# Kernel tuning notes

Measured on AMD Instinct MI355X. Metric: run time of the kernel, lower is better.

## Reference

```python
import jax, jax.numpy as jnp
import numpy as np
from math import sqrt

B, S, D, H = 4, 2048, 1024, 16
DH = D // H          # 64
DF = 4 * D           # 4096
EPS = 1e-5
NEG = -1e9


def layer_norm(x, w, b):
    mu = jnp.mean(x, axis=-1, keepdims=True)
    var = jnp.mean((x - mu) ** 2, axis=-1, keepdims=True)
    return (x - mu) * jax.lax.rsqrt(var + EPS) * w + b


def setup_inputs() -> dict:
    key = jax.random.key(0)
    ks = jax.random.split(key, 16)
    s = 0.02
    return {
        "state": jax.random.normal(ks[0], (B, S, D), jnp.float32),
        "mask": jax.random.randint(ks[1], (B, S), 0, 2, jnp.int32),
        "ln1_w": jnp.ones((D,), jnp.float32),
        "ln1_b": jnp.zeros((D,), jnp.float32),
        "Wq": jax.random.normal(ks[2], (H, D, DH), jnp.float32) * s,
        "bq": jnp.zeros((H, DH), jnp.float32),
        "Wk": jax.random.normal(ks[3], (H, D, DH), jnp.float32) * s,
        "bk": jnp.zeros((H, DH), jnp.float32),
        "Wv": jax.random.normal(ks[4], (H, D, DH), jnp.float32) * s,
        "bv": jnp.zeros((H, DH), jnp.float32),
        "Wo": jax.random.normal(ks[5], (D, D), jnp.float32) * s,
        "bo": jnp.zeros((D,), jnp.float32),
        "ln2_w": jnp.ones((D,), jnp.float32),
        "ln2_b": jnp.zeros((D,), jnp.float32),
        "W1": jax.random.normal(ks[6], (D, DF), jnp.float32) * s,
        "b1": jnp.zeros((DF,), jnp.float32),
        "W2": jax.random.normal(ks[7], (DF, D), jnp.float32) * s,
        "b2": jnp.zeros((D,), jnp.float32),
    }


def reference(state, mask, ln1_w, ln1_b, Wq, bq, Wk, bk, Wv, bv, Wo, bo,
              ln2_w, ln2_b, W1, b1, W2, b2):
    # pre-norm attention block
    hidden = layer_norm(state, ln1_w, ln1_b)               # [B,S,D]
    q = jnp.einsum("bsd,hde->bhse", hidden, Wq) + bq[None, :, None, :]
    k = jnp.einsum("bsd,hde->bhse", hidden, Wk) + bk[None, :, None, :]
    v = jnp.einsum("bsd,hde->bhse", hidden, Wv) + bv[None, :, None, :]
    scores = jnp.einsum("bhse,bhte->bhst", q, k) / sqrt(DH)  # [B,H,S,S]
    scores = jnp.where(mask[:, None, None, :] == 0, NEG, scores)
    weights = jax.nn.softmax(scores, axis=-1)
    attended = jnp.einsum("bhst,bhte->bhse", weights, v)    # [B,H,S,DH]
    # concat heads in head order (matches torch cat over per-head outputs)
    attended = attended.transpose(0, 2, 1, 3).reshape(B, S, D)
    attn_out = attended @ Wo + bo
    output = state + attn_out
    # pre-norm FFN block (dropout=0 -> identity)
    hidden = layer_norm(output, ln2_w, ln2_b)
    ff = jax.nn.gelu(hidden @ W1 + b1, approximate=False) @ W2 + b2
    return output + ff
```

## Files before the change

### kernel.cpp

```cpp
#include <hip/hip_runtime.h>
#include <math.h>

#define B_  4
#define S_  2048
#define D_  1024
#define H_  16
#define DH_ 64
#define DF_ 4096
#define M_  8192

typedef __attribute__((ext_vector_type(8))) short bf8_t;
typedef __attribute__((ext_vector_type(4))) short bf4_t;
typedef __attribute__((ext_vector_type(4))) float f4_t;

__device__ __forceinline__ unsigned short f2bf(float x) {
  union { float f; unsigned u; } v; v.f = x;
  unsigned r = v.u + 0x7fffu + ((v.u >> 16) & 1u);
  return (unsigned short)(r >> 16);
}

#if defined(__has_builtin)
#if __has_builtin(__builtin_amdgcn_cvt_pk_bf16_f32)
#define HAVE_PKCVT 1
#endif
#if __has_builtin(__builtin_amdgcn_mfma_f32_16x16x16bf16_1k)
#define HAVE_MFMA16 1
#endif
#if __has_builtin(__builtin_amdgcn_global_load_lds)
#define HAVE_ASYNC 1
#endif
#endif

__device__ __forceinline__ unsigned pk_bf16(float lo, float hi) {
#ifdef HAVE_PKCVT
  auto r = __builtin_amdgcn_cvt_pk_bf16_f32(lo, hi);
  unsigned u; __builtin_memcpy(&u, &r, 4); return u;
#else
  return (unsigned)f2bf(lo) | ((unsigned)f2bf(hi) << 16);
#endif
}

__device__ __forceinline__ bf4_t upk(unsigned u0, unsigned u1) {
  union { unsigned u[2]; bf4_t v; } c; c.u[0] = u0; c.u[1] = u1; return c.v;
}

__device__ __forceinline__ f4_t mfma32(bf8_t a, bf8_t b, f4_t c) {
  return __builtin_amdgcn_mfma_f32_16x16x32_bf16(a, b, c, 0, 0, 0);
}

__device__ __forceinline__ f4_t mfma16(bf4_t a, bf4_t b, f4_t c) {
#ifdef HAVE_MFMA16
  return __builtin_amdgcn_mfma_f32_16x16x16bf16_1k(a, b, c, 0, 0, 0);
#else
  bf8_t a8 = {a[0], a[1], a[2], a[3], 0, 0, 0, 0};
  bf8_t b8 = {b[0], b[1], b[2], b[3], 0, 0, 0, 0};
  return __builtin_amdgcn_mfma_f32_16x16x32_bf16(a8, b8, c, 0, 0, 0);
#endif
}

__device__ __forceinline__ void async16(const void* g, void* l) {
#ifdef HAVE_ASYNC
  __builtin_amdgcn_global_load_lds((__attribute__((address_space(1))) void*)(g),
                                   (__attribute__((address_space(3))) void*)(l), 16, 0, 0);
#else
  *(uint4*)l = *(const uint4*)g;
#endif
}

__device__ __forceinline__ int sw(int row) { return (row ^ (row >> 3)) & 7; }


__global__ __launch_bounds__(256) void wtrans_kernel(const float* __restrict__ in,
                                                     unsigned short* __restrict__ out,
                                                     int K, int N) {
  const int k0 = blockIdx.x * 32, n0 = blockIdx.y * 32;
  __shared__ float t[32][33];
  const int tid = threadIdx.x;
#pragma unroll
  for (int i = 0; i < 4; i++) {
    int idx = i * 256 + tid; int r = idx >> 5, c = idx & 31;
    t[r][c] = in[(size_t)(k0 + r) * N + n0 + c];
  }
  __syncthreads();
#pragma unroll
  for (int i = 0; i < 4; i++) {
    int idx = i * 256 + tid; int r = idx >> 5, c = idx & 31;
    out[(size_t)(n0 + r) * K + k0 + c] = f2bf(t[c][r]);
  }
}

__global__ __launch_bounds__(256) void qkvpack_kernel(const float* __restrict__ Wq,
                                                      const float* __restrict__ Wk,
                                                      const float* __restrict__ Wv,
                                                      unsigned short* __restrict__ WqkvT) {
  const int z = blockIdx.z;
  const int sel = z >> 4, h = z & 15;
  const float* in = (sel == 0 ? Wq : sel == 1 ? Wk : Wv) + (size_t)h * D_ * DH_;
  const int k0 = blockIdx.x * 32, n0 = blockIdx.y * 32;
  __shared__ float t[32][33];
  const int tid = threadIdx.x;
#pragma unroll
  for (int i = 0; i < 4; i++) {
    int idx = i * 256 + tid; int r = idx >> 5, c = idx & 31;
    t[r][c] = in[(size_t)(k0 + r) * DH_ + n0 + c];
  }
  __syncthreads();
#pragma unroll
  for (int i = 0; i < 4; i++) {
    int idx = i * 256 + tid; int r = idx >> 5, c = idx & 31;
    int n = sel * 1024 + h * 64 + n0 + r;
    WqkvT[(size_t)n * D_ + k0 + c] = f2bf(t[c][r]);
  }
}

__global__ void biaspack_kernel(const float* __restrict__ bq, const float* __restrict__ bk,
                                const float* __restrict__ bv, float* __restrict__ bqkv) {
  int i = blockIdx.x * 256 + threadIdx.x;
  if (i < 3072) {
    int sel = i >> 10, j = i & 1023;
    const float* src = sel == 0 ? bq : sel == 1 ? bk : bv;
    bqkv[i] = src[j];
  }
}


__global__ __launch_bounds__(256) void ln_kernel(const float* __restrict__ x,
                                                 const float* __restrict__ w,
                                                 const float* __restrict__ bb,
                                                 unsigned short* __restrict__ out) {
  const int row = blockIdx.x;
  const float* xr = x + (size_t)row * D_;
  const int tid = threadIdx.x;
  float v[4]; float s = 0.f;
#pragma unroll
  for (int i = 0; i < 4; i++) { v[i] = xr[tid + i * 256]; s += v[i]; }
  __shared__ float red[8];
#pragma unroll
  for (int o = 32; o; o >>= 1) s += __shfl_xor(s, o, 64);
  const int wv = tid >> 6, ln = tid & 63;
  if (!ln) red[wv] = s;
  __syncthreads();
  float mean = (red[0] + red[1] + red[2] + red[3]) * (1.f / 1024.f);
  float s2 = 0.f;
#pragma unroll
  for (int i = 0; i < 4; i++) { float d = v[i] - mean; s2 += d * d; }
#pragma unroll
  for (int o = 32; o; o >>= 1) s2 += __shfl_xor(s2, o, 64);
  if (!ln) red[4 + wv] = s2;
  __syncthreads();
  float var = (red[4] + red[5] + red[6] + red[7]) * (1.f / 1024.f);
  float rstd = rsqrtf(var + 1e-5f);
#pragma unroll
  for (int i = 0; i < 4; i++) {
    int c = tid + i * 256;
    out[(size_t)row * D_ + c] = f2bf((v[i] - mean) * rstd * w[c] + bb[c]);
  }
}

template <int EPI>
__global__ __launch_bounds__(256) void gemm_bt(const unsigned short* __restrict__ A,
                                               const unsigned short* __restrict__ Bt,
                                               const float* __restrict__ bias,
                                               const float* __restrict__ resid,
                                               unsigned short* __restrict__ outb,
                                               float* __restrict__ outf,
                                               int Ndim, int Kdim) {
  __shared__ __align__(16) unsigned short Asmem[4096];
  __shared__ __align__(16) unsigned short Bsmem[4096];
  const int tid = threadIdx.x;
  const int wave = tid >> 6, lane = tid & 63;
  const int quad = lane >> 4, l16 = lane & 15;
  const int wm = wave >> 1, wn = wave & 1;
  const int m0 = blockIdx.y * 128, n0 = blockIdx.x * 128;

  const f4_t fzero = {0.f, 0.f, 0.f, 0.f};
  f4_t acc[4][4];
#pragma unroll
  for (int i = 0; i < 4; i++)
#pragma unroll
    for (int j = 0; j < 4; j++) acc[i][j] = fzero;

  const int rowA = tid >> 2;
  const int kp = (tid & 3) * 8;

  for (int k0 = 0; k0 < Kdim; k0 += 32) {
    __syncthreads();
#pragma unroll
    for (int r = 0; r < 2; r++) {
      const int row = r * 64 + rowA;
      const int e = row * 32 + kp;
      async16(A  + (size_t)(m0 + row) * Kdim + k0 + kp, &Asmem[e]);
      async16(Bt + (size_t)(n0 + row) * Kdim + k0 + kp, &Bsmem[e]);
    }
    __syncthreads();

    bf8_t a[4], b[4];
#pragma unroll
    for (int i = 0; i < 4; i++) {
      a[i] = *(const bf8_t*)&Asmem[(wm * 64 + i * 16 + l16) * 32 + quad * 8];
      b[i] = *(const bf8_t*)&Bsmem[(wn * 64 + i * 16 + l16) * 32 + quad * 8];
    }
#pragma unroll
    for (int i = 0; i < 4; i++)
#pragma unroll
      for (int j = 0; j < 4; j++)
        acc[i][j] = mfma32(a[i], b[j], acc[i][j]);
  }

#pragma unroll
  for (int i = 0; i < 4; i++) {
#pragma unroll
    for (int j = 0; j < 4; j++) {
#pragma unroll
      for (int r = 0; r < 4; r++) {
        const int m = m0 + wm * 64 + i * 16 + quad * 4 + r;
        const int n = n0 + wn * 64 + j * 16 + l16;
        float v = acc[i][j][r] + bias[n];
        if constexpr (EPI == 2) v = 0.5f * v * (1.f + erff(v * 0.70710678118654752f));
        if constexpr (EPI == 1) {
          v += resid[(size_t)m * Ndim + n];
          outf[(size_t)m * Ndim + n] = v;
        } else {
          outb[(size_t)m * Ndim + n] = f2bf(v);
        }
      }
    }
  }
}


__global__ __launch_bounds__(256) void vtrans_kernel(const unsigned short* __restrict__ qkv,
                                                     unsigned short* __restrict__ vT) {
  const int bh = blockIdx.y, b = bh >> 4, h = bh & 15;
  const int t0 = blockIdx.x * 64;
  __shared__ unsigned short tile[64][65];
  const int tid = threadIdx.x;
#pragma unroll
  for (int i = 0; i < 16; i++) {
    int idx = i * 256 + tid;
    int t = idx >> 6, e = idx & 63;
    tile[e][t] = qkv[(size_t)(b * S_ + t0 + t) * 3072 + 2048 + h * 64 + e];
  }
  __syncthreads();
#pragma unroll
  for (int i = 0; i < 16; i++) {
    int idx = i * 256 + tid;
    int e = idx >> 6, t = idx & 63;
    vT[(size_t)(bh * 64 + e) * S_ + t0 + t] = tile[e][t];
  }
}


__global__ __launch_bounds__(256) void attn_kernel(const unsigned short* __restrict__ qkv,
                                                   const unsigned short* __restrict__ vT,
                                                   const int* __restrict__ maskp,
                                                   unsigned short* __restrict__ attended) {
  const int bh = blockIdx.y, b = bh >> 4, h = bh & 15;
  const int q0 = blockIdx.x * 128;
  const int tid = threadIdx.x, wv = tid >> 6, lane = tid & 63;
  const int quad = lane >> 4, l16 = lane & 15;
  __shared__ __align__(16) unsigned short smem[16640];
  __shared__ float biasl[64];
  unsigned short* Qs = smem;
  unsigned short* Ks = smem + 8192;
  unsigned short* Vs = smem + 12288;

#pragma unroll
  for (int r = 0; r < 4; r++) {
    int ci = r * 256 + tid;
    int row = ci >> 3, lc = (ci & 7) ^ sw(row);
    async16(qkv + (size_t)(b * S_ + q0 + row) * 3072 + h * 64 + lc * 8, &Qs[ci * 8]);
  }
  __syncthreads();
  bf8_t aq[2][2];
#pragma unroll
  for (int sb = 0; sb < 2; sb++) {
    int srow = wv * 32 + sb * 16 + l16;
    int sq = sw(srow);
    aq[sb][0] = *(const bf8_t*)&Qs[srow * 64 + (quad ^ sq) * 8];
    aq[sb][1] = *(const bf8_t*)&Qs[srow * 64 + ((quad + 4) ^ sq) * 8];
  }

  const f4_t fzero = {0.f, 0.f, 0.f, 0.f};
  f4_t o[2][4];
#pragma unroll
  for (int sb = 0; sb < 2; sb++)
#pragma unroll
    for (int ee = 0; ee < 4; ee++) o[sb][ee] = fzero;
  float lsum[2] = {0.f, 0.f};

  for (int t0 = 0; t0 < S_; t0 += 64) {
    __syncthreads();
#pragma unroll
    for (int r = 0; r < 2; r++) {
      int ci = r * 256 + tid;
      int row = ci >> 3, lc = (ci & 7) ^ sw(row);
      async16(qkv + (size_t)(b * S_ + t0 + row) * 3072 + 1024 + h * 64 + lc * 8, &Ks[ci * 8]);
      async16(vT + (size_t)(bh * 64 + row) * S_ + t0 + lc * 8, &Vs[ci * 8]);
    }
    if (tid < 64) biasl[tid] = maskp[b * S_ + t0 + tid] ? 0.f : -8e9f;
    __syncthreads();

    f4_t sf[2][4];
#pragma unroll
    for (int jj = 0; jj < 4; jj++) {
      f4_t bi = *(const f4_t*)&biasl[jj * 16 + quad * 4];
      sf[0][jj] = bi;
      sf[1][jj] = bi;
    }
#pragma unroll
    for (int jj = 0; jj < 4; jj++) {
      int krow = jj * 16 + l16, sk = sw(krow);
      bf8_t kf0 = *(const bf8_t*)&Ks[krow * 64 + (quad ^ sk) * 8];
      bf8_t kf1 = *(const bf8_t*)&Ks[krow * 64 + ((quad + 4) ^ sk) * 8];
      sf[0][jj] = mfma32(kf0, aq[0][0], sf[0][jj]);
      sf[0][jj] = mfma32(kf1, aq[0][1], sf[0][jj]);
      sf[1][jj] = mfma32(kf0, aq[1][0], sf[1][jj]);
      sf[1][jj] = mfma32(kf1, aq[1][1], sf[1][jj]);
    }

    unsigned pk[2][4][2];
#pragma unroll
    for (int sb = 0; sb < 2; sb++)
#pragma unroll
      for (int jj = 0; jj < 4; jj++) {
        float p0 = __expf(sf[sb][jj][0] * 0.125f);
        float p1 = __expf(sf[sb][jj][1] * 0.125f);
        float p2 = __expf(sf[sb][jj][2] * 0.125f);
        float p3 = __expf(sf[sb][jj][3] * 0.125f);
        lsum[sb] += (p0 + p1) + (p2 + p3);
        pk[sb][jj][0] = pk_bf16(p0, p1);
        pk[sb][jj][1] = pk_bf16(p2, p3);
      }

#pragma unroll
    for (int ee = 0; ee < 4; ee++) {
      int vrow = ee * 16 + l16, sv = sw(vrow);
#pragma unroll
      for (int jj = 0; jj < 4; jj++) {
        int lc2 = 2 * jj + (quad >> 1);
        bf4_t vf = *(const bf4_t*)&Vs[vrow * 64 + (lc2 ^ sv) * 8 + (quad & 1) * 4];
        o[0][ee] = mfma16(vf, upk(pk[0][jj][0], pk[0][jj][1]), o[0][ee]);
        o[1][ee] = mfma16(vf, upk(pk[1][jj][0], pk[1][jj][1]), o[1][ee]);
      }
    }
  }

#pragma unroll
  for (int sb = 0; sb < 2; sb++) {
    float l = lsum[sb];
    l += __shfl_xor(l, 16, 64);
    l += __shfl_xor(l, 32, 64);
    lsum[sb] = 1.f / l;
  }

  __syncthreads();
  unsigned short* Os = smem;
#pragma unroll
  for (int sb = 0; sb < 2; sb++) {
    int srow = wv * 32 + sb * 16 + l16;
#pragma unroll
    for (int ee = 0; ee < 4; ee++) {
      unsigned w0 = pk_bf16(o[sb][ee][0] * lsum[sb], o[sb][ee][1] * lsum[sb]);
      unsigned w1 = pk_bf16(o[sb][ee][2] * lsum[sb], o[sb][ee][3] * lsum[sb]);
      uint2 wq; wq.x = w0; wq.y = w1;
      *(uint2*)&Os[srow * 72 + ee * 16 + quad * 4] = wq;
    }
  }
  __syncthreads();
#pragma unroll
  for (int it = 0; it < 4; it++) {
    int row = it * 32 + (tid >> 3), e0 = (tid & 7) * 8;
    bf8_t v = *(const bf8_t*)&Os[row * 72 + e0];
    *(bf8_t*)&attended[(size_t)(b * S_ + q0 + row) * D_ + h * 64 + e0] = v;
  }
}


extern "C" void kernel_launch(void* const* d_in, const int* in_sizes, int n_in,
                              void* d_out, int out_size, void* d_ws, size_t ws_size,
                              hipStream_t stream) {
  const float* state = (const float*)d_in[0];
  const int*   maskp = (const int*)d_in[1];
  const float* ln1w  = (const float*)d_in[2];
  const float* ln1b  = (const float*)d_in[3];
  const float* Wq    = (const float*)d_in[4];
  const float* bq    = (const float*)d_in[5];
  const float* Wk    = (const float*)d_in[6];
  const float* bk    = (const float*)d_in[7];
  const float* Wv    = (const float*)d_in[8];
  const float* bv    = (const float*)d_in[9];
  const float* Wo    = (const float*)d_in[10];
  const float* bo    = (const float*)d_in[11];
  const float* ln2w  = (const float*)d_in[12];
  const float* ln2b  = (const float*)d_in[13];
  const float* W1    = (const float*)d_in[14];
  const float* b1    = (const float*)d_in[15];
  const float* W2    = (const float*)d_in[16];
  const float* b2    = (const float*)d_in[17];

  char* w = (char*)d_ws;
  unsigned short* hidden = (unsigned short*)w; w += (size_t)M_ * D_ * 2;
  unsigned short* qkv    = (unsigned short*)w; w += (size_t)M_ * 3072 * 2;
  unsigned short* vT     = (unsigned short*)w; w += (size_t)M_ * D_ * 2;
  float*          outp   = (float*)w;          w += (size_t)M_ * D_ * 4;
  unsigned short* WqkvT  = (unsigned short*)w; w += (size_t)3072 * D_ * 2;
  unsigned short* WoT    = (unsigned short*)w; w += (size_t)D_ * D_ * 2;
  unsigned short* W1T    = (unsigned short*)w; w += (size_t)DF_ * D_ * 2;
  unsigned short* W2T    = (unsigned short*)w; w += (size_t)D_ * DF_ * 2;
  float*          bqkv   = (float*)w;          w += 3072 * 4;
  unsigned short* ff1    = qkv;

  qkvpack_kernel<<<dim3(32, 2, 48), 256, 0, stream>>>(Wq, Wk, Wv, WqkvT);
  wtrans_kernel<<<dim3(32, 32), 256, 0, stream>>>(Wo, WoT, D_, D_);
  wtrans_kernel<<<dim3(32, 128), 256, 0, stream>>>(W1, W1T, D_, DF_);
  wtrans_kernel<<<dim3(128, 32), 256, 0, stream>>>(W2, W2T, DF_, D_);
  biaspack_kernel<<<12, 256, 0, stream>>>(bq, bk, bv, bqkv);

  ln_kernel<<<M_, 256, 0, stream>>>(state, ln1w, ln1b, hidden);
  gemm_bt<0><<<dim3(3072 / 128, M_ / 128), 256, 0, stream>>>(hidden, WqkvT, bqkv, nullptr,
                                                             qkv, nullptr, 3072, D_);
  vtrans_kernel<<<dim3(S_ / 64, B_ * H_), 256, 0, stream>>>(qkv, vT);
  attn_kernel<<<dim3(S_ / 128, B_ * H_), 256, 0, stream>>>(qkv, vT, maskp, hidden);
  gemm_bt<1><<<dim3(D_ / 128, M_ / 128), 256, 0, stream>>>(hidden, WoT, bo, state,
                                                           nullptr, outp, D_, D_);
  ln_kernel<<<M_, 256, 0, stream>>>(outp, ln2w, ln2b, hidden);
  gemm_bt<2><<<dim3(DF_ / 128, M_ / 128), 256, 0, stream>>>(hidden, W1T, b1, nullptr,
                                                            ff1, nullptr, DF_, D_);
  gemm_bt<1><<<dim3(D_ / 128, M_ / 128), 256, 0, stream>>>(ff1, W2T, b2, outp,
                                                           nullptr, (float*)d_out, D_, DF_);
}
```

Before: 630.9 us.

## Fold softmax scale into Q projection, use K=32 MFMA for PV and row sums

The Q projection epilogue now multiplies Q by log2(e)/sqrt(dh), so the attention loop can use exp2f with no per-element scale. V^T is written with a permuted column order so that PV can use the 16x16x32 bf16 MFMA with 8-wide P fragments instead of the 16x16x16 variant. Softmax row sums are computed by an MFMA against a ones vector, which replaces the scalar adds and cross-lane shuffles. Q is loaded straight from global memory into registers, dropping the Q LDS stage and one barrier and cutting LDS size. Summing the bf16-rounded probabilities slightly changes numerics, and correctness depends on the permutation matching the MFMA operand layout.

```diff
diff --git a/kernel.cpp b/kernel.cpp
--- a/kernel.cpp
+++ b/kernel.cpp
@@ -9,8 +9,9 @@
 #define DF_ 4096
 #define M_  8192
 
+#define QSC 0.18033688011112042f
+
 typedef __attribute__((ext_vector_type(8))) short bf8_t;
-typedef __attribute__((ext_vector_type(4))) short bf4_t;
 typedef __attribute__((ext_vector_type(4))) float f4_t;
 
 __device__ __forceinline__ unsigned short f2bf(float x) {
@@ -22,9 +23,6 @@
 #if defined(__has_builtin)
 #if __has_builtin(__builtin_amdgcn_cvt_pk_bf16_f32)
 #define HAVE_PKCVT 1
-#endif
-#if __has_builtin(__builtin_amdgcn_mfma_f32_16x16x16bf16_1k)
-#define HAVE_MFMA16 1
 #endif
 #if __has_builtin(__builtin_amdgcn_global_load_lds)
 #define HAVE_ASYNC 1
@@ -40,22 +38,13 @@
 #endif
 }
 
-__device__ __forceinline__ bf4_t upk(unsigned u0, unsigned u1) {
-  union { unsigned u[2]; bf4_t v; } c; c.u[0] = u0; c.u[1] = u1; return c.v;
+__device__ __forceinline__ bf8_t upk8(unsigned u0, unsigned u1, unsigned u2, unsigned u3) {
+  union { unsigned u[4]; bf8_t v; } c;
+  c.u[0] = u0; c.u[1] = u1; c.u[2] = u2; c.u[3] = u3; return c.v;
 }
 
 __device__ __forceinline__ f4_t mfma32(bf8_t a, bf8_t b, f4_t c) {
   return __builtin_amdgcn_mfma_f32_16x16x32_bf16(a, b, c, 0, 0, 0);
-}
-
-__device__ __forceinline__ f4_t mfma16(bf4_t a, bf4_t b, f4_t c) {
-#ifdef HAVE_MFMA16
-  return __builtin_amdgcn_mfma_f32_16x16x16bf16_1k(a, b, c, 0, 0, 0);
-#else
-  bf8_t a8 = {a[0], a[1], a[2], a[3], 0, 0, 0, 0};
-  bf8_t b8 = {b[0], b[1], b[2], b[3], 0, 0, 0, 0};
-  return __builtin_amdgcn_mfma_f32_16x16x32_bf16(a8, b8, c, 0, 0, 0);
-#endif
 }
 
 __device__ __forceinline__ void async16(const void* g, void* l) {
@@ -207,6 +196,7 @@
         acc[i][j] = mfma32(a[i], b[j], acc[i][j]);
   }
 
+  const float sc = (EPI == 0 && n0 < 1024) ? QSC : 1.f;
 #pragma unroll
   for (int i = 0; i < 4; i++) {
 #pragma unroll
@@ -216,6 +206,7 @@
         const int m = m0 + wm * 64 + i * 16 + quad * 4 + r;
         const int n = n0 + wn * 64 + j * 16 + l16;
         float v = acc[i][j][r] + bias[n];
+        if constexpr (EPI == 0) v *= sc;
         if constexpr (EPI == 2) v = 0.5f * v * (1.f + erff(v * 0.70710678118654752f));
         if constexpr (EPI == 1) {
           v += resid[(size_t)m * Ndim + n];
@@ -246,7 +237,8 @@
   for (int i = 0; i < 16; i++) {
     int idx = i * 256 + tid;
     int e = idx >> 6, t = idx & 63;
-    vT[(size_t)(bh * 64 + e) * S_ + t0 + t] = tile[e][t];
+    int gt = (t & 32) + 8 * ((t >> 2) & 3) + 4 * ((t >> 4) & 1) + (t & 3);
+    vT[(size_t)(bh * 64 + e) * S_ + t0 + gt] = tile[e][t];
   }
 }
 
@@ -259,35 +251,29 @@
   const int q0 = blockIdx.x * 128;
   const int tid = threadIdx.x, wv = tid >> 6, lane = tid & 63;
   const int quad = lane >> 4, l16 = lane & 15;
-  __shared__ __align__(16) unsigned short smem[16640];
+  __shared__ __align__(16) unsigned short smem[9216];
   __shared__ float biasl[64];
-  unsigned short* Qs = smem;
-  unsigned short* Ks = smem + 8192;
-  unsigned short* Vs = smem + 12288;
-
-#pragma unroll
-  for (int r = 0; r < 4; r++) {
-    int ci = r * 256 + tid;
-    int row = ci >> 3, lc = (ci & 7) ^ sw(row);
-    async16(qkv + (size_t)(b * S_ + q0 + row) * 3072 + h * 64 + lc * 8, &Qs[ci * 8]);
-  }
-  __syncthreads();
+  unsigned short* Ks = smem;
+  unsigned short* Vs = smem + 4096;
+
   bf8_t aq[2][2];
 #pragma unroll
   for (int sb = 0; sb < 2; sb++) {
-    int srow = wv * 32 + sb * 16 + l16;
-    int sq = sw(srow);
-    aq[sb][0] = *(const bf8_t*)&Qs[srow * 64 + (quad ^ sq) * 8];
-    aq[sb][1] = *(const bf8_t*)&Qs[srow * 64 + ((quad + 4) ^ sq) * 8];
-  }
-
+    const unsigned short* qrow =
+        qkv + (size_t)(b * S_ + q0 + wv * 32 + sb * 16 + l16) * 3072 + h * 64;
+    aq[sb][0] = *(const bf8_t*)(qrow + quad * 8);
+    aq[sb][1] = *(const bf8_t*)(qrow + 32 + quad * 8);
+  }
+
+  const bf8_t ones8 = {0x3F80, 0x3F80, 0x3F80, 0x3F80, 0x3F80, 0x3F80, 0x3F80, 0x3F80};
   const f4_t fzero = {0.f, 0.f, 0.f, 0.f};
-  f4_t o[2][4];
-#pragma unroll
-  for (int sb = 0; sb < 2; sb++)
+  f4_t o[2][4], lacc[2];
+#pragma unroll
+  for (int sb = 0; sb < 2; sb++) {
+    lacc[sb] = fzero;
 #pragma unroll
     for (int ee = 0; ee < 4; ee++) o[sb][ee] = fzero;
-  float lsum[2] = {0.f, 0.f};
+  }
 
   for (int t0 = 0; t0 < S_; t0 += 64) {
     __syncthreads();
@@ -319,40 +305,37 @@
       sf[1][jj] = mfma32(kf1, aq[1][1], sf[1][jj]);
     }
 
-    unsigned pk[2][4][2];
-#pragma unroll
-    for (int sb = 0; sb < 2; sb++)
-#pragma unroll
-      for (int jj = 0; jj < 4; jj++) {
-        float p0 = __expf(sf[sb][jj][0] * 0.125f);
-        float p1 = __expf(sf[sb][jj][1] * 0.125f);
-        float p2 = __expf(sf[sb][jj][2] * 0.125f);
-        float p3 = __expf(sf[sb][jj][3] * 0.125f);
-        lsum[sb] += (p0 + p1) + (p2 + p3);
-        pk[sb][jj][0] = pk_bf16(p0, p1);
-        pk[sb][jj][1] = pk_bf16(p2, p3);
+    bf8_t pp[2][2];
+#pragma unroll
+    for (int sb = 0; sb < 2; sb++) {
+#pragma unroll
+      for (int h2 = 0; h2 < 2; h2++) {
+        float p0 = exp2f(sf[sb][2 * h2][0]),     p1 = exp2f(sf[sb][2 * h2][1]);
+        float p2 = exp2f(sf[sb][2 * h2][2]),     p3 = exp2f(sf[sb][2 * h2][3]);
+        float p4 = exp2f(sf[sb][2 * h2 + 1][0]), p5 = exp2f(sf[sb][2 * h2 + 1][1]);
+        float p6 = exp2f(sf[sb][2 * h2 + 1][2]), p7 = exp2f(sf[sb][2 * h2 + 1][3]);
+        pp[sb][h2] = upk8(pk_bf16(p0, p1), pk_bf16(p2, p3),
+                          pk_bf16(p4, p5), pk_bf16(p6, p7));
       }
+      lacc[sb] = mfma32(ones8, pp[sb][0], lacc[sb]);
+      lacc[sb] = mfma32(ones8, pp[sb][1], lacc[sb]);
+    }
 
 #pragma unroll
     for (int ee = 0; ee < 4; ee++) {
       int vrow = ee * 16 + l16, sv = sw(vrow);
 #pragma unroll
-      for (int jj = 0; jj < 4; jj++) {
-        int lc2 = 2 * jj + (quad >> 1);
-        bf4_t vf = *(const bf4_t*)&Vs[vrow * 64 + (lc2 ^ sv) * 8 + (quad & 1) * 4];
-        o[0][ee] = mfma16(vf, upk(pk[0][jj][0], pk[0][jj][1]), o[0][ee]);
-        o[1][ee] = mfma16(vf, upk(pk[1][jj][0], pk[1][jj][1]), o[1][ee]);
+      for (int h2 = 0; h2 < 2; h2++) {
+        bf8_t vf = *(const bf8_t*)&Vs[vrow * 64 + ((4 * h2 + quad) ^ sv) * 8];
+        o[0][ee] = mfma32(vf, pp[0][h2], o[0][ee]);
+        o[1][ee] = mfma32(vf, pp[1][h2], o[1][ee]);
       }
     }
   }
 
-#pragma unroll
-  for (int sb = 0; sb < 2; sb++) {
-    float l = lsum[sb];
-    l += __shfl_xor(l, 16, 64);
-    l += __shfl_xor(l, 32, 64);
-    lsum[sb] = 1.f / l;
-  }
+  float linv[2];
+#pragma unroll
+  for (int sb = 0; sb < 2; sb++) linv[sb] = 1.f / lacc[sb][0];
 
   __syncthreads();
   unsigned short* Os = smem;
@@ -361,8 +344,8 @@
     int srow = wv * 32 + sb * 16 + l16;
 #pragma unroll
     for (int ee = 0; ee < 4; ee++) {
-      unsigned w0 = pk_bf16(o[sb][ee][0] * lsum[sb], o[sb][ee][1] * lsum[sb]);
-      unsigned w1 = pk_bf16(o[sb][ee][2] * lsum[sb], o[sb][ee][3] * lsum[sb]);
+      unsigned w0 = pk_bf16(o[sb][ee][0] * linv[sb], o[sb][ee][1] * linv[sb]);
+      unsigned w1 = pk_bf16(o[sb][ee][2] * linv[sb], o[sb][ee][3] * linv[sb]);
       uint2 wq; wq.x = w0; wq.y = w1;
       *(uint2*)&Os[srow * 72 + ee * 16 + quad * 4] = wq;
     }
```

Result: slower. 655.1 us (+3.8%).
